# Optimization experiments

Measured on AMD Instinct MI355X. Metric: run time of the kernel, lower is better.

## Reference

```python
import jax, jax.numpy as jnp
import numpy as np

DIM = 768
HEADS = 12
T_TOK = 4  # num_frames // tubelet_size
EPS = 1e-6


def _layernorm(x, w, b):
    m = jnp.mean(x, axis=-1, keepdims=True)
    v = jnp.var(x, axis=-1, keepdims=True)
    return (x - m) * jax.lax.rsqrt(v + EPS) * w + b


def _conv1d(g, w, b):
    # g: (Bv, C, T), w: (C_out, C_in, 3) torch layout, padding=1
    y = jax.lax.conv_general_dilated(g, w, window_strides=(1,), padding=[(1, 1)],
                                     dimension_numbers=("NCH", "OIH", "NCH"))
    return y + b[None, :, None]


def setup_inputs() -> dict:
    key = jax.random.key(0)
    ks = jax.random.split(key, 16)
    D, F = DIM, DIM * 4
    s = 0.02
    return {
        "x": jax.random.normal(ks[0], (64, 197, D), jnp.float32),
        "ln1_w": jnp.ones((D,), jnp.float32),
        "ln1_b": jnp.zeros((D,), jnp.float32),
        "qkv_w": jax.random.normal(ks[1], (3 * D, D), jnp.float32) * s,
        "qkv_b": jnp.zeros((3 * D,), jnp.float32),
        "convq_w": jax.random.normal(ks[2], (D, D, 3), jnp.float32) * s,
        "convq_b": jnp.zeros((D,), jnp.float32),
        "convk_w": jax.random.normal(ks[3], (D, D, 3), jnp.float32) * s,
        "convk_b": jnp.zeros((D,), jnp.float32),
        "proj_w": jax.random.normal(ks[4], (D, D), jnp.float32) * s,
        "proj_b": jnp.zeros((D,), jnp.float32),
        "ln2_w": jnp.ones((D,), jnp.float32),
        "ln2_b": jnp.zeros((D,), jnp.float32),
        "ff1_w": jax.random.normal(ks[5], (F, D), jnp.float32) * s,
        "ff1_b": jnp.zeros((F,), jnp.float32),
        "ff2_w": jax.random.normal(ks[6], (D, F), jnp.float32) * s,
        "ff2_b": jnp.zeros((D,), jnp.float32),
    }


def reference(x, ln1_w, ln1_b, qkv_w, qkv_b, convq_w, convq_b, convk_w, convk_b,
              proj_w, proj_b, ln2_w, ln2_b, ff1_w, ff1_b, ff2_w, ff2_b):
    B, N, C = x.shape
    H, Dh = HEADS, C // HEADS

    # --- attention branch ---
    h = _layernorm(x, ln1_w, ln1_b)
    # temporal context from per-frame CLS tokens
    g = h[:, 0, :].reshape(B // T_TOK, T_TOK, C).transpose(0, 2, 1)  # (Bv, C, T)
    cq = _conv1d(g, convq_w, convq_b).transpose(0, 2, 1).reshape(B, H, 1, Dh)
    ck = _conv1d(g, convk_w, convk_b).transpose(0, 2, 1).reshape(B, H, 1, Dh)

    qkv = (h @ qkv_w.T + qkv_b).reshape(B, N, 3, H, Dh).transpose(2, 0, 3, 1, 4)
    q, k, v = qkv[0], qkv[1], qkv[2]  # (B, H, N, Dh)

    scale = Dh ** -0.5
    scores = jnp.einsum("bhnd,bhmd->bhnm", q + cq, k + ck) * scale
    attn = jax.nn.softmax(scores, axis=-1)
    o = jnp.einsum("bhnm,bhmd->bhnd", attn, v)
    o = o.transpose(0, 2, 1, 3).reshape(B, N, C)
    o = o @ proj_w.T + proj_b
    x = x + o

    # --- FFN branch ---
    h2 = _layernorm(x, ln2_w, ln2_b)
    h2 = jax.nn.gelu(h2 @ ff1_w.T + ff1_b, approximate=False)
    x = x + (h2 @ ff2_w.T + ff2_b)
    return x
```

## Files before the change

### kernel.cpp

```cpp
#include <hip/hip_runtime.h>
#include <hip/hip_bf16.h>


typedef __attribute__((ext_vector_type(8))) short  short8;
typedef __attribute__((ext_vector_type(4))) float  float4v;
typedef __attribute__((ext_vector_type(4))) unsigned short ushort4v;
typedef unsigned short ushort;

#define DEV static __device__ __forceinline__

DEV ushort f2bf(float f) {
  union { float f; unsigned u; } v; v.f = f;
  unsigned r = v.u + 0x7fffu + ((v.u >> 16) & 1u);
  return (ushort)(r >> 16);
}
DEV float bf2f(ushort h) {
  union { unsigned u; float f; } v; v.u = ((unsigned)h) << 16;
  return v.f;
}

DEV void gld_lds16(const void* g, void* l) {
  __builtin_amdgcn_global_load_lds(
      (const __attribute__((address_space(1))) void*)g,
      (__attribute__((address_space(3))) void*)l, 16, 0, 0);
}

__global__ void wcvt(const float* __restrict__ in, ushort* __restrict__ out, int n4) {
  int i = blockIdx.x * 256 + threadIdx.x;
  if (i >= n4) return;
  float4 f = *((const float4*)in + i);
  ushort4v o;
  o[0] = f2bf(f.x); o[1] = f2bf(f.y); o[2] = f2bf(f.z); o[3] = f2bf(f.w);
  *(ushort4v*)(out + (size_t)i * 4) = o;
}

__global__ __launch_bounds__(256) void ln_k(const float* __restrict__ x,
                                            const float* __restrict__ w,
                                            const float* __restrict__ b,
                                            ushort* __restrict__ out) {
  int wid = threadIdx.x >> 6, lane = threadIdx.x & 63;
  int row = blockIdx.x * 4 + wid;
  size_t base = (size_t)row * 768;
  const float4* xr = (const float4*)(x + base);
  const float4* w4 = (const float4*)w;
  const float4* b4 = (const float4*)b;
  float4 v[3];
  float s = 0.f, q = 0.f;
#pragma unroll
  for (int j = 0; j < 3; ++j) {
    v[j] = xr[j * 64 + lane];
    s += v[j].x + v[j].y + v[j].z + v[j].w;
    q += v[j].x * v[j].x + v[j].y * v[j].y + v[j].z * v[j].z + v[j].w * v[j].w;
  }
#pragma unroll
  for (int m = 1; m < 64; m <<= 1) { s += __shfl_xor(s, m); q += __shfl_xor(q, m); }
  float mean = s * (1.f / 768.f);
  float var  = q * (1.f / 768.f) - mean * mean;
  float rstd = rsqrtf(var + 1e-6f);
  ushort* orow = out + base;
#pragma unroll
  for (int j = 0; j < 3; ++j) {
    float4 wv = w4[j * 64 + lane], bv = b4[j * 64 + lane];
    ushort4v o;
    o[0] = f2bf((v[j].x - mean) * rstd * wv.x + bv.x);
    o[1] = f2bf((v[j].y - mean) * rstd * wv.y + bv.y);
    o[2] = f2bf((v[j].z - mean) * rstd * wv.z + bv.z);
    o[3] = f2bf((v[j].w - mean) * rstd * wv.w + bv.w);
    *(ushort4v*)(orow + (size_t)(j * 64 + lane) * 4) = o;
  }
}

__global__ __launch_bounds__(256) void conv_cls(const ushort* __restrict__ h,
                                                const float* __restrict__ wq,
                                                const float* __restrict__ wk,
                                                float* __restrict__ cq,
                                                float* __restrict__ ck) {
  __shared__ float gsh[16][6][48];
  int tid = threadIdx.x;
  int cc = blockIdx.x;
  int kc = blockIdx.y;
  for (int idx = tid; idx < 16 * 2 * 48; idx += 256) {
    int ci = idx % 48; int t = (idx / 48) & 1; int v = idx / 96;
    gsh[v][t * 5][ci] = 0.f;
  }
  for (int idx = tid; idx < 16 * 4 * 48; idx += 256) {
    int ci = idx % 48; int t = (idx / 48) & 3; int v = idx / 192;
    gsh[v][t + 1][ci] = bf2f(h[(size_t)(v * 4 + t) * 197 * 768 + kc * 48 + ci]);
  }
  __syncthreads();
  int cl = tid >> 2, t = tid & 3;
  int cout = cc * 64 + cl;
  const float* wqp = wq + ((size_t)cout * 768 + kc * 48) * 3;
  const float* wkp = wk + ((size_t)cout * 768 + kc * 48) * 3;
  float aq[16] = {}, ak[16] = {};
  for (int ci = 0; ci < 48; ++ci) {
    float q0 = wqp[ci * 3], q1 = wqp[ci * 3 + 1], q2 = wqp[ci * 3 + 2];
    float k0 = wkp[ci * 3], k1 = wkp[ci * 3 + 1], k2 = wkp[ci * 3 + 2];
#pragma unroll
    for (int v = 0; v < 16; ++v) {
      float g0 = gsh[v][t][ci], g1 = gsh[v][t + 1][ci], g2 = gsh[v][t + 2][ci];
      aq[v] += q0 * g0 + q1 * g1 + q2 * g2;
      ak[v] += k0 * g0 + k1 * g1 + k2 * g2;
    }
  }
#pragma unroll
  for (int v = 0; v < 16; ++v) {
    atomicAdd(&cq[(size_t)(v * 4 + t) * 768 + cout], aq[v]);
    atomicAdd(&ck[(size_t)(v * 4 + t) * 768 + cout], ak[v]);
  }
}

template <int EPI>
__global__ __launch_bounds__(512, 2) void gemm256(
    const ushort* __restrict__ A, const ushort* __restrict__ W,
    int M, int N, int K, int mt, const float* __restrict__ bias,
    float* __restrict__ out_f, ushort* __restrict__ out_h,
    const float* __restrict__ res,
    const float* __restrict__ cq, const float* __restrict__ ck,
    const float* __restrict__ cqb, const float* __restrict__ ckb,
    ushort* __restrict__ Qo, ushort* __restrict__ Ko, ushort* __restrict__ Vo) {
  __shared__ ushort As[2][256 * 64];
  __shared__ ushort Bs[2][256 * 64];

  int nwg = gridDim.x;
  int bid = blockIdx.x;
  int q8 = nwg >> 3, r8 = nwg & 7;
  int xcd = bid & 7, idx = bid >> 3;
  int wg = (xcd < r8 ? xcd * (q8 + 1) : r8 * (q8 + 1) + (xcd - r8) * q8) + idx;
  int tileCol = wg / mt;
  int tileRow = wg - tileCol * mt;

  long rowBase = (long)tileRow * 256;
  int  colBase = tileCol * 256;

  int tid = threadIdx.x;
  int wid = tid >> 6, lane = tid & 63;
  int wr = wid >> 2, wc = wid & 3;
  int cG = lane >> 4, cl = lane & 15;

  const ushort* asrc[4];
  const ushort* wsrc[4];
  int dstoff[4];
#pragma unroll
  for (int j = 0; j < 4; ++j) {
    int flat = j * 512 + tid;
    int r = flat >> 3, c = flat & 7;
    long ar = rowBase + r; if (ar > M - 1) ar = M - 1;
    asrc[j] = A + ar * (size_t)K + (c ^ (r & 7)) * 8;
    wsrc[j] = W + (size_t)(colBase + r) * K + (c ^ (r & 7)) * 8;
    dstoff[j] = flat * 8;
  }

  float4v acc[8][4] = {};

#pragma unroll
  for (int j = 0; j < 4; ++j) {
    gld_lds16(asrc[j], &As[0][0] + dstoff[j]);
    gld_lds16(wsrc[j], &Bs[0][0] + dstoff[j]);
  }
  __syncthreads();

  int nt = K >> 6;
  for (int t = 0; t < nt; ++t) {
    const ushort* as = &As[t & 1][0];
    const ushort* bs = &Bs[t & 1][0];
    if (t + 1 < nt) {
      ushort* an = &As[(t + 1) & 1][0];
      ushort* bn = &Bs[(t + 1) & 1][0];
      int kt = (t + 1) << 6;
#pragma unroll
      for (int j = 0; j < 4; ++j) {
        gld_lds16(asrc[j] + kt, an + dstoff[j]);
        gld_lds16(wsrc[j] + kt, bn + dstoff[j]);
      }
    }
#pragma unroll
    for (int ks = 0; ks < 2; ++ks) {
      short8 bfv[4];
#pragma unroll
      for (int fj = 0; fj < 4; ++fj) {
        int r = wc * 64 + fj * 16 + cl;
        bfv[fj] = *(const short8*)(bs + r * 64 + (((ks << 2) | cG) ^ (r & 7)) * 8);
      }
#pragma unroll
      for (int fi = 0; fi < 8; ++fi) {
        int r = wr * 128 + fi * 16 + cl;
        short8 av = *(const short8*)(as + r * 64 + (((ks << 2) | cG) ^ (r & 7)) * 8);
#pragma unroll
        for (int fj = 0; fj < 4; ++fj)
          acc[fi][fj] = __builtin_amdgcn_mfma_f32_16x16x32_bf16(av, bfv[fj], acc[fi][fj], 0, 0, 0);
      }
    }
    __syncthreads();
  }

#pragma unroll
  for (int fi = 0; fi < 8; ++fi) {
    long r0 = rowBase + wr * 128 + fi * 16 + 4 * cG;
#pragma unroll
    for (int fj = 0; fj < 4; ++fj) {
      int col = colBase + wc * 64 + fj * 16 + cl;
      float bc = bias[col];
      float4v a = acc[fi][fj];
#pragma unroll
      for (int j = 0; j < 4; ++j) {
        long row = r0 + j;
        if (row >= M) continue;
        float v = a[j] + bc;
        if constexpr (EPI == 0) {
          int sec = col / 768; int ccc = col - sec * 768;
          int bi = (int)(row / 197); int ni = (int)(row - (long)bi * 197);
          size_t oidx = ((size_t)(bi * 12 + (ccc >> 6)) * 197 + ni) * 64 + (ccc & 63);
          if (sec == 0)      { v += cq[bi * 768 + ccc] + cqb[ccc]; Qo[oidx] = f2bf(v); }
          else if (sec == 1) { v += ck[bi * 768 + ccc] + ckb[ccc]; Ko[oidx] = f2bf(v); }
          else               { Vo[oidx] = f2bf(v); }
        } else if constexpr (EPI == 1 || EPI == 3) {
          size_t idx = (size_t)row * N + col;
          out_f[idx] = v + res[idx];
        } else {
          size_t idx = (size_t)row * N + col;
          float g = 0.5f * v * (1.0f + erff(v * 0.70710678118f));
          out_h[idx] = f2bf(g);
        }
      }
    }
  }
}

__global__ __launch_bounds__(256, 2) void attn_k(const ushort* __restrict__ Q,
                                                 const ushort* __restrict__ Kg,
                                                 const ushort* __restrict__ Vg,
                                                 ushort* __restrict__ O) {
  __shared__ ushort Ks[224 * 64];
  __shared__ ushort Vt[64 * 224];
  __shared__ ushort Ps[4][16 * 40];
  int g = blockIdx.x;
  int bi = g / 12, hh = g - bi * 12;
  size_t gbase = (size_t)g * 197 * 64;
  int tid = threadIdx.x, wid = tid >> 6, lane = tid & 63;
  int cG = lane >> 4, cl = lane & 15;

  {
    int rr = tid >> 3, ch = tid & 7;
#pragma unroll
    for (int i = 0; i < 7; ++i) {
      int n = rr + 32 * i;
      short8 kv = {0, 0, 0, 0, 0, 0, 0, 0};
      if (n < 197) kv = *(const short8*)(Kg + gbase + (size_t)n * 64 + ch * 8);
      *(short8*)(Ks + n * 64 + (ch ^ (n & 7)) * 8) = kv;
      short8 vv = {0, 0, 0, 0, 0, 0, 0, 0};
      if (n < 197) vv = *(const short8*)(Vg + gbase + (size_t)n * 64 + ch * 8);
#pragma unroll
      for (int j = 0; j < 8; ++j) {
        int dd = ch * 8 + j;
        Vt[dd * 224 + (n ^ ((dd & 7) << 3))] = ((ushort*)&vv)[j];
      }
    }
  }
  __syncthreads();

  for (int rt = wid; rt < 13; rt += 4) {
    int nq = rt * 16 + cl; if (nq > 196) nq = 196;
    short8 aq0 = *(const short8*)(Q + gbase + (size_t)nq * 64 + 8 * cG);
    short8 aq1 = *(const short8*)(Q + gbase + (size_t)nq * 64 + 32 + 8 * cG);
    float4v s[14];
#pragma unroll
    for (int ct = 0; ct < 14; ++ct) {
      float4v a = {0.f, 0.f, 0.f, 0.f};
      int np = ct * 16 + cl;
      short8 b0 = *(const short8*)(Ks + np * 64 + ((cG    ) ^ (np & 7)) * 8);
      short8 b1 = *(const short8*)(Ks + np * 64 + ((4 + cG) ^ (np & 7)) * 8);
      a = __builtin_amdgcn_mfma_f32_16x16x32_bf16(aq0, b0, a, 0, 0, 0);
      a = __builtin_amdgcn_mfma_f32_16x16x32_bf16(aq1, b1, a, 0, 0, 0);
      s[ct] = a;
    }
    float mx[4] = {-1e30f, -1e30f, -1e30f, -1e30f};
#pragma unroll
    for (int ct = 0; ct < 14; ++ct) {
      int colv = ct * 16 + cl;
#pragma unroll
      for (int j = 0; j < 4; ++j) {
        float v = (colv < 197) ? s[ct][j] * 0.125f : -1e30f;
        s[ct][j] = v;
        mx[j] = fmaxf(mx[j], v);
      }
    }
#pragma unroll
    for (int m = 1; m < 16; m <<= 1)
#pragma unroll
      for (int j = 0; j < 4; ++j) mx[j] = fmaxf(mx[j], __shfl_xor(mx[j], m));
    float sum[4] = {0.f, 0.f, 0.f, 0.f};
#pragma unroll
    for (int ct = 0; ct < 14; ++ct)
#pragma unroll
      for (int j = 0; j < 4; ++j) {
        float p = __expf(s[ct][j] - mx[j]);
        s[ct][j] = p;
        sum[j] += p;
      }
#pragma unroll
    for (int m = 1; m < 16; m <<= 1)
#pragma unroll
      for (int j = 0; j < 4; ++j) sum[j] += __shfl_xor(sum[j], m);
    float rs[4];
#pragma unroll
    for (int j = 0; j < 4; ++j) rs[j] = 1.0f / sum[j];

    float4v oa[4] = {};
    ushort* P = &Ps[wid][0];
#pragma unroll
    for (int ks = 0; ks < 7; ++ks) {
#pragma unroll
      for (int t = 0; t < 2; ++t) {
        int ct = 2 * ks + t;
#pragma unroll
        for (int j = 0; j < 4; ++j)
          P[(4 * cG + j) * 40 + t * 16 + cl] = f2bf(s[ct][j]);
      }
      short8 pa = *(const short8*)(P + cl * 40 + 8 * cG);
#pragma unroll
      for (int dt = 0; dt < 4; ++dt) {
        int dd = dt * 16 + cl;
        short8 bv = *(const short8*)(Vt + dd * 224 + ((ks * 32 + 8 * cG) ^ ((dd & 7) << 3)));
        oa[dt] = __builtin_amdgcn_mfma_f32_16x16x32_bf16(pa, bv, oa[dt], 0, 0, 0);
      }
    }
#pragma unroll
    for (int dt = 0; dt < 4; ++dt)
#pragma unroll
      for (int j = 0; j < 4; ++j) {
        int n2 = rt * 16 + 4 * cG + j;
        if (n2 < 197)
          O[(size_t)(bi * 197 + n2) * 768 + hh * 64 + dt * 16 + cl] = f2bf(oa[dt][j] * rs[j]);
      }
  }
}

extern "C" void kernel_launch(void* const* d_in, const int* in_sizes, int n_in,
                              void* d_out, int out_size, void* d_ws, size_t ws_size,
                              hipStream_t stream) {
  const float* x     = (const float*)d_in[0];
  const float* ln1w  = (const float*)d_in[1];
  const float* ln1b  = (const float*)d_in[2];
  const float* qkvw  = (const float*)d_in[3];
  const float* qkvb  = (const float*)d_in[4];
  const float* cqw   = (const float*)d_in[5];
  const float* cqb   = (const float*)d_in[6];
  const float* ckw   = (const float*)d_in[7];
  const float* ckb   = (const float*)d_in[8];
  const float* projw = (const float*)d_in[9];
  const float* projb = (const float*)d_in[10];
  const float* ln2w  = (const float*)d_in[11];
  const float* ln2b  = (const float*)d_in[12];
  const float* ff1w  = (const float*)d_in[13];
  const float* ff1b  = (const float*)d_in[14];
  const float* ff2w  = (const float*)d_in[15];
  const float* ff2b  = (const float*)d_in[16];
  float* out = (float*)d_out;

  char* ws = (char*)d_ws;
  const size_t SZ = (size_t)12608 * 768 * 2;
  ushort* Qb  = (ushort*)(ws);
  ushort* Kb  = (ushort*)(ws + SZ);
  ushort* Vb  = (ushort*)(ws + 2 * SZ);
  ushort* Ob  = (ushort*)(ws + 3 * SZ);
  ushort* ffh = (ushort*)(ws);
  ushort* hb  = (ushort*)(ws + 4 * SZ);
  float* x1 = (float*)(ws + 5 * SZ);
  float* cq = (float*)(ws + 5 * SZ + (size_t)12608 * 768 * 4);
  float* ck = cq + 49152;
  ushort* Wqkv  = (ushort*)(ck + 49152);
  ushort* Wproj = Wqkv + 1769472;
  ushort* Wff1  = Wproj + 589824;
  ushort* Wff2  = Wff1 + 2359296;

  wcvt<<<1728, 256, 0, stream>>>(qkvw, Wqkv, 442368);
  wcvt<<<576,  256, 0, stream>>>(projw, Wproj, 147456);
  wcvt<<<2304, 256, 0, stream>>>(ff1w, Wff1, 589824);
  wcvt<<<2304, 256, 0, stream>>>(ff2w, Wff2, 589824);

  ln_k<<<3152, 256, 0, stream>>>(x, ln1w, ln1b, hb);

  hipMemsetAsync(cq, 0, 2 * 49152 * sizeof(float), stream);
  conv_cls<<<dim3(12, 16), 256, 0, stream>>>(hb, cqw, ckw, cq, ck);

  gemm256<0><<<450, 512, 0, stream>>>(hb, Wqkv, 12608, 2304, 768, 50, qkvb,
      nullptr, nullptr, nullptr, cq, ck, cqb, ckb, Qb, Kb, Vb);

  attn_k<<<768, 256, 0, stream>>>(Qb, Kb, Vb, Ob);

  gemm256<1><<<150, 512, 0, stream>>>(Ob, Wproj, 12608, 768, 768, 50, projb,
      x1, nullptr, x, nullptr, nullptr, nullptr, nullptr, nullptr, nullptr, nullptr);

  ln_k<<<3152, 256, 0, stream>>>(x1, ln2w, ln2b, hb);

  gemm256<2><<<600, 512, 0, stream>>>(hb, Wff1, 12608, 3072, 768, 50, ff1b,
      nullptr, ffh, nullptr, nullptr, nullptr, nullptr, nullptr, nullptr, nullptr, nullptr);

  gemm256<3><<<150, 512, 0, stream>>>(ffh, Wff2, 12608, 768, 3072, 50, ff2b,
      out, nullptr, x1, nullptr, nullptr, nullptr, nullptr, nullptr, nullptr, nullptr);
}
```

Before: 697.4 us.

## Rewrite bf16 GEMM main loop as an eight-phase interleaved load/MFMA pipeline

The GEMM inner loop is replaced with a schedule that splits each 256x64 tile into 128-row halves. It processes two K-tiles per iteration in eight phases, each issuing a few LDS fragment reads and one global-to-LDS prefetch and then a block of MFMAs. Explicit vmcnt/lgkmcnt waits, s_barrier and s_setprio replace the coarse __syncthreads-per-tile pattern, so global loads, LDS reads and matrix math overlap more tightly. The row clamp on A loads is dropped, so the last tile row reads past M into neighbouring workspace memory. Those rows are still masked in the epilogue, but the correctness now relies on that. The schedule also assumes K is a multiple of 128.

Measured after the change: 744.6 us. 1.07x slower.

```diff
diff --git a/kernel.cpp b/kernel.cpp
--- a/kernel.cpp
+++ b/kernel.cpp
@@ -110,8 +110,39 @@
   }
 }
 
+#define PH_BAR() __builtin_amdgcn_s_barrier()
+#define LGKM0() do { asm volatile("s_waitcnt lgkmcnt(0)" ::: "memory"); \
+                     __builtin_amdgcn_sched_barrier(0); } while (0)
+#define VMC2() do { asm volatile("s_waitcnt vmcnt(2)" ::: "memory"); \
+                    __builtin_amdgcn_sched_barrier(0); } while (0)
+#define VMC0() do { asm volatile("s_waitcnt vmcnt(0)" ::: "memory"); \
+                    __builtin_amdgcn_sched_barrier(0); } while (0)
+
+#define RDA(P, fb) do { _Pragma("unroll") for (int f = 0; f < 4; ++f) { \
+    af[0][f] = *(const short8*)((P) + ((fb) + f) * 1024 + swz0); \
+    af[1][f] = *(const short8*)((P) + ((fb) + f) * 1024 + swz1); } } while (0)
+
+#define RDB(P, gb, BF) do { _Pragma("unroll") for (int g = 0; g < 2; ++g) { \
+    BF[0][g] = *(const short8*)((P) + ((gb) + g) * 1024 + swz0); \
+    BF[1][g] = *(const short8*)((P) + ((gb) + g) * 1024 + swz1); } } while (0)
+
+#define MMQ(fb, gb, BF) do { __builtin_amdgcn_s_setprio(1); \
+    _Pragma("unroll") for (int f = 0; f < 4; ++f) { \
+      _Pragma("unroll") for (int g = 0; g < 2; ++g) { \
+        acc[(fb)+f][(gb)+g] = __builtin_amdgcn_mfma_f32_16x16x32_bf16(af[0][f], BF[0][g], acc[(fb)+f][(gb)+g], 0, 0, 0); \
+        acc[(fb)+f][(gb)+g] = __builtin_amdgcn_mfma_f32_16x16x32_bf16(af[1][f], BF[1][g], acc[(fb)+f][(gb)+g], 0, 0, 0); \
+      } } \
+    __builtin_amdgcn_s_setprio(0); } while (0)
+
+#define STGA(tile, h) do { \
+    gld_lds16(A + aoff[0][h] + (long)(tile) * 64, &LA[(tile) & 1][h][fl0]); \
+    gld_lds16(A + aoff[1][h] + (long)(tile) * 64, &LA[(tile) & 1][h][fl1]); } while (0)
+#define STGB(tile, h) do { \
+    gld_lds16(W + boff[0][h] + (long)(tile) * 64, &LB[(tile) & 1][h][fl0]); \
+    gld_lds16(W + boff[1][h] + (long)(tile) * 64, &LB[(tile) & 1][h][fl1]); } while (0)
+
 template <int EPI>
-__global__ __launch_bounds__(512, 2) void gemm256(
+__global__ __launch_bounds__(512, 2) void gemm8p(
     const ushort* __restrict__ A, const ushort* __restrict__ W,
     int M, int N, int K, int mt, const float* __restrict__ bias,
     float* __restrict__ out_f, ushort* __restrict__ out_h,
@@ -119,8 +150,8 @@
     const float* __restrict__ cq, const float* __restrict__ ck,
     const float* __restrict__ cqb, const float* __restrict__ ckb,
     ushort* __restrict__ Qo, ushort* __restrict__ Ko, ushort* __restrict__ Vo) {
-  __shared__ ushort As[2][256 * 64];
-  __shared__ ushort Bs[2][256 * 64];
+  __shared__ ushort LA[2][2][8192];
+  __shared__ ushort LB[2][2][8192];
 
   int nwg = gridDim.x;
   int bid = blockIdx.x;
@@ -138,60 +169,60 @@
   int wr = wid >> 2, wc = wid & 3;
   int cG = lane >> 4, cl = lane & 15;
 
-  const ushort* asrc[4];
-  const ushort* wsrc[4];
-  int dstoff[4];
-#pragma unroll
-  for (int j = 0; j < 4; ++j) {
+  long aoff[2][2], boff[2][2];
+#pragma unroll
+  for (int j = 0; j < 2; ++j) {
     int flat = j * 512 + tid;
     int r = flat >> 3, c = flat & 7;
-    long ar = rowBase + r; if (ar > M - 1) ar = M - 1;
-    asrc[j] = A + ar * (size_t)K + (c ^ (r & 7)) * 8;
-    wsrc[j] = W + (size_t)(colBase + r) * K + (c ^ (r & 7)) * 8;
-    dstoff[j] = flat * 8;
-  }
-
+    long co = (long)((c ^ (r & 7)) * 8);
+#pragma unroll
+    for (int h = 0; h < 2; ++h) {
+      aoff[j][h] = (long)(rowBase + h * 128 + r) * K + co;
+      boff[j][h] = (long)(colBase + h * 128 + r) * K + co;
+    }
+  }
+  int fl0 = tid * 8, fl1 = (512 + tid) * 8;
+
+  const ushort* pA0 = &LA[0][wr][0] + cl * 64;
+  const ushort* pA1 = &LA[1][wr][0] + cl * 64;
+  const ushort* pB0 = &LB[0][wc >> 1][0] + ((wc & 1) * 64 + cl) * 64;
+  const ushort* pB1 = &LB[1][wc >> 1][0] + ((wc & 1) * 64 + cl) * 64;
+  int swz0 = ((cG) ^ (cl & 7)) * 8;
+  int swz1 = ((4 + cG) ^ (cl & 7)) * 8;
+
+  short8 af[2][4], bf0[2][2], bf1[2][2];
   float4v acc[8][4] = {};
 
-#pragma unroll
-  for (int j = 0; j < 4; ++j) {
-    gld_lds16(asrc[j], &As[0][0] + dstoff[j]);
-    gld_lds16(wsrc[j], &Bs[0][0] + dstoff[j]);
-  }
-  __syncthreads();
-
-  int nt = K >> 6;
-  for (int t = 0; t < nt; ++t) {
-    const ushort* as = &As[t & 1][0];
-    const ushort* bs = &Bs[t & 1][0];
-    if (t + 1 < nt) {
-      ushort* an = &As[(t + 1) & 1][0];
-      ushort* bn = &Bs[(t + 1) & 1][0];
-      int kt = (t + 1) << 6;
-#pragma unroll
-      for (int j = 0; j < 4; ++j) {
-        gld_lds16(asrc[j] + kt, an + dstoff[j]);
-        gld_lds16(wsrc[j] + kt, bn + dstoff[j]);
-      }
-    }
-#pragma unroll
-    for (int ks = 0; ks < 2; ++ks) {
-      short8 bfv[4];
-#pragma unroll
-      for (int fj = 0; fj < 4; ++fj) {
-        int r = wc * 64 + fj * 16 + cl;
-        bfv[fj] = *(const short8*)(bs + r * 64 + (((ks << 2) | cG) ^ (r & 7)) * 8);
-      }
-#pragma unroll
-      for (int fi = 0; fi < 8; ++fi) {
-        int r = wr * 128 + fi * 16 + cl;
-        short8 av = *(const short8*)(as + r * 64 + (((ks << 2) | cG) ^ (r & 7)) * 8);
-#pragma unroll
-        for (int fj = 0; fj < 4; ++fj)
-          acc[fi][fj] = __builtin_amdgcn_mfma_f32_16x16x32_bf16(av, bfv[fj], acc[fi][fj], 0, 0, 0);
-      }
-    }
-    __syncthreads();
+  STGA(0, 0); STGA(0, 1); STGB(0, 0); STGB(0, 1); STGA(1, 0);
+  VMC2();
+  PH_BAR();
+
+  int NI = K >> 7;
+  for (int it = 0; it < NI; ++it) {
+    int t1 = 2 * it + 1, t2 = 2 * it + 2, t3 = 2 * it + 3;
+    bool more = (it + 1 < NI);
+    RDA(pA0, 0); RDB(pB0, 0, bf0);
+    STGB(t1, 0);
+    PH_BAR(); LGKM0(); MMQ(0, 0, bf0); PH_BAR();
+    RDB(pB0, 2, bf1);
+    STGB(t1, 1);
+    PH_BAR(); LGKM0(); MMQ(0, 2, bf1); PH_BAR();
+    RDA(pA0, 4);
+    STGA(t1, 1);
+    PH_BAR(); LGKM0(); MMQ(4, 2, bf1); PH_BAR();
+    if (more) { STGA(t2, 0); VMC2(); } else { VMC0(); }
+    PH_BAR(); LGKM0(); MMQ(4, 0, bf0); PH_BAR();
+    RDA(pA1, 0); RDB(pB1, 0, bf0);
+    if (more) STGA(t2, 1);
+    PH_BAR(); LGKM0(); MMQ(0, 0, bf0); PH_BAR();
+    RDB(pB1, 2, bf1);
+    if (more) STGB(t2, 0);
+    PH_BAR(); LGKM0(); MMQ(0, 2, bf1); PH_BAR();
+    RDA(pA1, 4);
+    if (more) STGB(t2, 1);
+    PH_BAR(); LGKM0(); MMQ(4, 2, bf1); PH_BAR();
+    if (more) { STGA(t3, 0); VMC2(); } else { VMC0(); }
+    PH_BAR(); LGKM0(); MMQ(4, 0, bf0); PH_BAR();
   }
 
 #pragma unroll
@@ -384,19 +415,19 @@
   hipMemsetAsync(cq, 0, 2 * 49152 * sizeof(float), stream);
   conv_cls<<<dim3(12, 16), 256, 0, stream>>>(hb, cqw, ckw, cq, ck);
 
-  gemm256<0><<<450, 512, 0, stream>>>(hb, Wqkv, 12608, 2304, 768, 50, qkvb,
+  gemm8p<0><<<450, 512, 0, stream>>>(hb, Wqkv, 12608, 2304, 768, 50, qkvb,
       nullptr, nullptr, nullptr, cq, ck, cqb, ckb, Qb, Kb, Vb);
 
   attn_k<<<768, 256, 0, stream>>>(Qb, Kb, Vb, Ob);
 
-  gemm256<1><<<150, 512, 0, stream>>>(Ob, Wproj, 12608, 768, 768, 50, projb,
+  gemm8p<1><<<150, 512, 0, stream>>>(Ob, Wproj, 12608, 768, 768, 50, projb,
       x1, nullptr, x, nullptr, nullptr, nullptr, nullptr, nullptr, nullptr, nullptr);
 
   ln_k<<<3152, 256, 0, stream>>>(x1, ln2w, ln2b, hb);
 
-  gemm256<2><<<600, 512, 0, stream>>>(hb, Wff1, 12608, 3072, 768, 50, ff1b,
+  gemm8p<2><<<600, 512, 0, stream>>>(hb, Wff1, 12608, 3072, 768, 50, ff1b,
       nullptr, ffh, nullptr, nullptr, nullptr, nullptr, nullptr, nullptr, nullptr, nullptr);
 
-  gemm256<3><<<150, 512, 0, stream>>>(ffh, Wff2, 12608, 768, 3072, 50, ff2b,
+  gemm8p<3><<<150, 512, 0, stream>>>(ffh, Wff2, 12608, 768, 3072, 50, ff2b,
       out, nullptr, x1, nullptr, nullptr, nullptr, nullptr, nullptr, nullptr, nullptr);
 }
```

## Shrink GEMM tiles to 128x128 single-buffered and use tanh GELU approximation

Applied to the files above, without the earlier changes.

Replaces the 256x256 double-buffered 512-thread GEMM with a 128x128 single-buffered 256-thread tile, giving about four times as many workgroups. The aim is better occupancy and less wave quantization on 256 CUs, especially for the narrow N=768 projection and FF2 GEMMs that previously launched only 150 blocks. This gives up prefetch overlap and per-tile reuse. Separately, exact erf GELU is replaced by a tanh-based approximation using fast exp, which changes numerics slightly.

New measurement: 579.4 us. 1.2x faster.

```diff
diff --git a/kernel.cpp b/kernel.cpp
--- a/kernel.cpp
+++ b/kernel.cpp
@@ -23,6 +23,13 @@
   __builtin_amdgcn_global_load_lds(
       (const __attribute__((address_space(1))) void*)g,
       (__attribute__((address_space(3))) void*)l, 16, 0, 0);
+}
+
+DEV float gelu_f(float v) {
+  float u = v * (0.7978845608f + 0.0356774081f * v * v);
+  float e = __expf(2.0f * u);
+  float t = 1.0f - __fdividef(2.0f, e + 1.0f);
+  return 0.5f * v * (1.0f + t);
 }
 
 __global__ void wcvt(const float* __restrict__ in, ushort* __restrict__ out, int n4) {
@@ -111,7 +118,7 @@
 }
 
 template <int EPI>
-__global__ __launch_bounds__(512, 2) void gemm256(
+__global__ __launch_bounds__(256, 2) void gemm_k(
     const ushort* __restrict__ A, const ushort* __restrict__ W,
     int M, int N, int K, int mt, const float* __restrict__ bias,
     float* __restrict__ out_f, ushort* __restrict__ out_h,
@@ -119,84 +126,73 @@
     const float* __restrict__ cq, const float* __restrict__ ck,
     const float* __restrict__ cqb, const float* __restrict__ ckb,
     ushort* __restrict__ Qo, ushort* __restrict__ Ko, ushort* __restrict__ Vo) {
-  __shared__ ushort As[2][256 * 64];
-  __shared__ ushort Bs[2][256 * 64];
+  __shared__ ushort As[128 * 64];
+  __shared__ ushort Bs[128 * 64];
 
   int nwg = gridDim.x;
   int bid = blockIdx.x;
   int q8 = nwg >> 3, r8 = nwg & 7;
-  int xcd = bid & 7, idx = bid >> 3;
-  int wg = (xcd < r8 ? xcd * (q8 + 1) : r8 * (q8 + 1) + (xcd - r8) * q8) + idx;
+  int xcd = bid & 7, sub = bid >> 3;
+  int wg = (xcd < r8 ? xcd * (q8 + 1) : r8 * (q8 + 1) + (xcd - r8) * q8) + sub;
   int tileCol = wg / mt;
   int tileRow = wg - tileCol * mt;
 
-  long rowBase = (long)tileRow * 256;
-  int  colBase = tileCol * 256;
+  long rowBase = (long)tileRow * 128;
+  int  colBase = tileCol * 128;
 
   int tid = threadIdx.x;
   int wid = tid >> 6, lane = tid & 63;
-  int wr = wid >> 2, wc = wid & 3;
+  int wr = wid >> 1, wc = wid & 1;
   int cG = lane >> 4, cl = lane & 15;
 
   const ushort* asrc[4];
   const ushort* wsrc[4];
-  int dstoff[4];
+  int dsto[4];
 #pragma unroll
   for (int j = 0; j < 4; ++j) {
-    int flat = j * 512 + tid;
+    int flat = j * 256 + tid;
     int r = flat >> 3, c = flat & 7;
     long ar = rowBase + r; if (ar > M - 1) ar = M - 1;
-    asrc[j] = A + ar * (size_t)K + (c ^ (r & 7)) * 8;
-    wsrc[j] = W + (size_t)(colBase + r) * K + (c ^ (r & 7)) * 8;
-    dstoff[j] = flat * 8;
-  }
-
-  float4v acc[8][4] = {};
-
-#pragma unroll
-  for (int j = 0; j < 4; ++j) {
-    gld_lds16(asrc[j], &As[0][0] + dstoff[j]);
-    gld_lds16(wsrc[j], &Bs[0][0] + dstoff[j]);
-  }
-  __syncthreads();
-
-  int nt = K >> 6;
-  for (int t = 0; t < nt; ++t) {
-    const ushort* as = &As[t & 1][0];
-    const ushort* bs = &Bs[t & 1][0];
-    if (t + 1 < nt) {
-      ushort* an = &As[(t + 1) & 1][0];
-      ushort* bn = &Bs[(t + 1) & 1][0];
-      int kt = (t + 1) << 6;
-#pragma unroll
-      for (int j = 0; j < 4; ++j) {
-        gld_lds16(asrc[j] + kt, an + dstoff[j]);
-        gld_lds16(wsrc[j] + kt, bn + dstoff[j]);
-      }
-    }
+    long co = (long)((c ^ (r & 7)) * 8);
+    asrc[j] = A + ar * (size_t)K + co;
+    wsrc[j] = W + (size_t)(colBase + r) * K + co;
+    dsto[j] = flat * 8;
+  }
+
+  float4v acc[4][4] = {};
+
+  for (int kt = 0; kt < K; kt += 64) {
+    __syncthreads();
+#pragma unroll
+    for (int j = 0; j < 4; ++j) {
+      gld_lds16(asrc[j] + kt, As + dsto[j]);
+      gld_lds16(wsrc[j] + kt, Bs + dsto[j]);
+    }
+    __syncthreads();
 #pragma unroll
     for (int ks = 0; ks < 2; ++ks) {
-      short8 bfv[4];
+      short8 af[4], bfr[4];
+#pragma unroll
+      for (int fi = 0; fi < 4; ++fi) {
+        int r = wr * 64 + fi * 16 + cl;
+        af[fi] = *(const short8*)(As + r * 64 + ((((ks << 2) | cG) ^ (r & 7)) * 8));
+      }
 #pragma unroll
       for (int fj = 0; fj < 4; ++fj) {
         int r = wc * 64 + fj * 16 + cl;
-        bfv[fj] = *(const short8*)(bs + r * 64 + (((ks << 2) | cG) ^ (r & 7)) * 8);
-      }
-#pragma unroll
-      for (int fi = 0; fi < 8; ++fi) {
-        int r = wr * 128 + fi * 16 + cl;
-        short8 av = *(const short8*)(as + r * 64 + (((ks << 2) | cG) ^ (r & 7)) * 8);
+        bfr[fj] = *(const short8*)(Bs + r * 64 + ((((ks << 2) | cG) ^ (r & 7)) * 8));
+      }
+#pragma unroll
+      for (int fi = 0; fi < 4; ++fi)
 #pragma unroll
         for (int fj = 0; fj < 4; ++fj)
-          acc[fi][fj] = __builtin_amdgcn_mfma_f32_16x16x32_bf16(av, bfv[fj], acc[fi][fj], 0, 0, 0);
-      }
-    }
-    __syncthreads();
-  }
-
-#pragma unroll
-  for (int fi = 0; fi < 8; ++fi) {
-    long r0 = rowBase + wr * 128 + fi * 16 + 4 * cG;
+          acc[fi][fj] = __builtin_amdgcn_mfma_f32_16x16x32_bf16(af[fi], bfr[fj], acc[fi][fj], 0, 0, 0);
+    }
+  }
+
+#pragma unroll
+  for (int fi = 0; fi < 4; ++fi) {
+    long r0 = rowBase + wr * 64 + fi * 16 + 4 * cG;
 #pragma unroll
     for (int fj = 0; fj < 4; ++fj) {
       int col = colBase + wc * 64 + fj * 16 + cl;
@@ -219,8 +215,7 @@
           out_f[idx] = v + res[idx];
         } else {
           size_t idx = (size_t)row * N + col;
-          float g = 0.5f * v * (1.0f + erff(v * 0.70710678118f));
-          out_h[idx] = f2bf(g);
+          out_h[idx] = f2bf(gelu_f(v));
         }
       }
     }
@@ -384,19 +379,19 @@
   hipMemsetAsync(cq, 0, 2 * 49152 * sizeof(float), stream);
   conv_cls<<<dim3(12, 16), 256, 0, stream>>>(hb, cqw, ckw, cq, ck);
 
-  gemm256<0><<<450, 512, 0, stream>>>(hb, Wqkv, 12608, 2304, 768, 50, qkvb,
+  gemm_k<0><<<1782, 256, 0, stream>>>(hb, Wqkv, 12608, 2304, 768, 99, qkvb,
       nullptr, nullptr, nullptr, cq, ck, cqb, ckb, Qb, Kb, Vb);
 
   attn_k<<<768, 256, 0, stream>>>(Qb, Kb, Vb, Ob);
 
-  gemm256<1><<<150, 512, 0, stream>>>(Ob, Wproj, 12608, 768, 768, 50, projb,
+  gemm_k<1><<<594, 256, 0, stream>>>(Ob, Wproj, 12608, 768, 768, 99, projb,
       x1, nullptr, x, nullptr, nullptr, nullptr, nullptr, nullptr, nullptr, nullptr);
 
   ln_k<<<3152, 256, 0, stream>>>(x1, ln2w, ln2b, hb);
 
-  gemm256<2><<<600, 512, 0, stream>>>(hb, Wff1, 12608, 3072, 768, 50, ff1b,
+  gemm_k<2><<<2376, 256, 0, stream>>>(hb, Wff1, 12608, 3072, 768, 99, ff1b,
       nullptr, ffh, nullptr, nullptr, nullptr, nullptr, nullptr, nullptr, nullptr, nullptr);
 
-  gemm256<3><<<150, 512, 0, stream>>>(ffh, Wff2, 12608, 768, 3072, 50, ff2b,
+  gemm_k<3><<<594, 256, 0, stream>>>(ffh, Wff2, 12608, 768, 3072, 99, ff2b,
       out, nullptr, x1, nullptr, nullptr, nullptr, nullptr, nullptr, nullptr, nullptr);
 }
```
